# Optimization experiments

Hardware: AMD Instinct MI355X
Metric: run time of the kernel (lower is better)

Reference implementation:

```python
import jax, jax.numpy as jnp
import numpy as np

VNUMS = [4248, 4258, 5327, 3721, 5404, 2818]
B, C, H, W = 12, 64, 192, 192
DV, HID, BOX = 128, 256, 32


def _roi_patches(imgs, pros, imgbatch, box_len=BOX):
    # torchvision roi_align (aligned=False, sampling_ratio -> 1 sample per 1x1 bin):
    # bilinear sample at bin centers x1 + (j+0.5), y1 + (i+0.5)
    ar = jnp.arange(box_len, dtype=pros.dtype) + 0.5
    xs = pros[:, 0:1] - box_len / 2.0 + ar  # [G, box]
    ys = pros[:, 1:2] - box_len / 2.0 + ar  # [G, box]
    img_g = imgs[imgbatch]  # [G, C, H, W]

    def sample_one(img_chw, ys1, xs1):
        yy, xx = jnp.meshgrid(ys1, xs1, indexing="ij")  # [box, box]
        def per_c(ch):
            return jax.scipy.ndimage.map_coordinates(ch, [yy, xx], order=1, mode="nearest")
        return jax.vmap(per_c)(img_chw)  # [C, box, box]

    return jax.vmap(sample_one)(img_g, ys, xs)  # [G, C, box, box]


def setup_inputs() -> dict:
    key = jax.random.key(0)
    ks = jax.random.split(key, 6)
    G = 2 * B
    gtypes = np.array([(g // 2) % 6 if g % 2 == 0 else ((g // 2) + 3) % 6 for g in range(G)], dtype=np.int64)
    vnums_g = np.array([VNUMS[t] for t in gtypes])
    off = np.concatenate([[0], np.cumsum(vnums_g)])
    Nv = int(off[-1])  # 103104
    gar_of_vert = np.repeat(np.arange(G), vnums_g)
    idxs = []
    for t in range(6):
        gl = np.nonzero(gtypes == t)[0]
        idxs.append(np.concatenate([off[g] + np.arange(VNUMS[t]) for g in gl]).astype(np.int32))
    Din = DV + C
    pros = jax.random.uniform(ks[1], (G, 2), jnp.float32) * (H - 2.0 * BOX) + BOX
    inp = {
        "imgs": jax.random.normal(ks[0], (B, C, H, W), jnp.float32),
        "pros": pros,
        "x_verts": jax.random.normal(ks[2], (Nv, DV), jnp.float32),
        "W1": jax.random.normal(ks[3], (6, Din, HID), jnp.float32) / np.sqrt(Din).astype(np.float32),
        "W2": jax.random.normal(ks[4], (6, HID, HID), jnp.float32) / np.sqrt(HID).astype(np.float32),
        "W3": jax.random.normal(ks[5], (6, HID, 3), jnp.float32) / np.sqrt(HID).astype(np.float32),
        "imgbatch": jnp.asarray(np.arange(G) // 2, jnp.int32),
        "gar_of_vert": jnp.asarray(gar_of_vert, jnp.int32),
    }
    for t in range(6):
        inp[f"idx_t{t}"] = jnp.asarray(idxs[t])
    return inp


def reference(imgs, pros, x_verts, W1, W2, W3, imgbatch, gar_of_vert,
              idx_t0, idx_t1, idx_t2, idx_t3, idx_t4, idx_t5):
    # 1) roi_align patch extraction + pooled per-garment image feature
    patches = _roi_patches(imgs, pros, imgbatch)        # [G, C, 32, 32]
    garf = patches.mean(axis=(2, 3))                     # [G, C]
    # 2) per-vertex feature = [vertex feat | garment image feat]
    feat = jnp.concatenate([x_verts, garf[gar_of_vert]], axis=-1)  # [Nv, DV+C]
    # 3) MoE-style dispatch per garment type -> per-type expert MLP -> scatter-combine
    out = jnp.zeros((x_verts.shape[0], 3), feat.dtype)
    for t, idx in enumerate([idx_t0, idx_t1, idx_t2, idx_t3, idx_t4, idx_t5]):
        ft = feat[idx]                                   # gather (dispatch)
        h = jax.nn.relu(ft @ W1[t])
        h = jax.nn.relu(h @ W2[t])
        out = out.at[idx].set(h @ W3[t])                 # scatter (combine)
    return out
```

## Files before the change

### kernel.cpp

```cpp
#include <hip/hip_runtime.h>

typedef __attribute__((ext_vector_type(8))) short short8;
typedef __attribute__((ext_vector_type(4))) float float4_;

__device__ __forceinline__ unsigned short f2bf(float f) {
    unsigned u = __float_as_uint(f);
    u += 0x7FFFu + ((u >> 16) & 1u);
    return (unsigned short)(u >> 16);
}

#define GARF_BLOCKS 1536
#define PREP_BLOCKS 2784

__global__ void prep_garf(const float* __restrict__ imgs,
                          const float* __restrict__ pros,
                          const int* __restrict__ imgbatch,
                          const float* __restrict__ W1,
                          const float* __restrict__ W2,
                          const float* __restrict__ W3,
                          unsigned short* __restrict__ w1t,
                          unsigned short* __restrict__ w2t,
                          unsigned short* __restrict__ w3t,
                          float* __restrict__ garf) {
    const int tid = threadIdx.x;
    if (blockIdx.x < GARF_BLOCKS) {
        __shared__ float part[4];
        int pc = blockIdx.x;
        int g = pc >> 6, c = pc & 63;
        int b = imgbatch[g];
        float cx = pros[g * 2 + 0], cy = pros[g * 2 + 1];
        int i = tid >> 3;
        int j0 = (tid & 7) * 4;
        float y = cy - 16.0f + (float)i + 0.5f;
        float yf = floorf(y);
        float wy1 = y - yf, wy0 = 1.0f - wy1;
        int iy0 = min(max((int)yf, 0), 191), iy1 = min(max((int)yf + 1, 0), 191);
        const float* base = imgs + (size_t)(b * 64 + c) * 36864;
        const float* r0 = base + iy0 * 192;
        const float* r1 = base + iy1 * 192;
        float sum = 0.0f;
#pragma unroll
        for (int jj = 0; jj < 4; ++jj) {
            float x = cx - 16.0f + (float)(j0 + jj) + 0.5f;
            float xf = floorf(x);
            float wx1 = x - xf, wx0 = 1.0f - wx1;
            int ix0 = min(max((int)xf, 0), 191), ix1 = min(max((int)xf + 1, 0), 191);
            sum += wy0 * (wx0 * r0[ix0] + wx1 * r0[ix1]) +
                   wy1 * (wx0 * r1[ix0] + wx1 * r1[ix1]);
        }
        for (int s = 32; s >= 1; s >>= 1) sum += __shfl_xor(sum, s);
        if ((tid & 63) == 0) part[tid >> 6] = sum;
        __syncthreads();
        if (tid == 0)
            garf[g * 64 + c] = (part[0] + part[1] + part[2] + part[3]) * (1.0f / 1024.0f);
    } else {
        int id = (blockIdx.x - GARF_BLOCKS) * 256 + tid;
        if (id < 294912) {
            int t = id / 49152, r = id % 49152;
            int k = r >> 8, n = r & 255;
            w1t[t * 49152 + n * 192 + k] = f2bf(W1[id]);
        } else if (id < 688128) {
            int i2 = id - 294912;
            int t = i2 >> 16, r = i2 & 65535;
            int k = r >> 8, n = r & 255;
            w2t[t * 65536 + n * 256 + k] = f2bf(W2[i2]);
        } else if (id < 712704) {
            int i3 = id - 688128;
            int t = i3 >> 12, r = i3 & 4095;
            int n = r >> 8, k = r & 255;
            w3t[i3] = (n < 3) ? f2bf(W3[t * 768 + k * 3 + n]) : (unsigned short)0;
        }
    }
}

struct MoEArgs {
    const float* x_verts;
    const int* gar;
    const int* idx[6];
    const unsigned short* w1t;
    const unsigned short* w2t;
    const unsigned short* w3t;
    const float* garf;
    float* out;
    int cnt[6];
    int tile_end[6];
};

__global__ __launch_bounds__(512, 4) void moe_kernel(MoEArgs a) {
    __shared__ __align__(16) char smem[2][32768];

    const int tid = threadIdx.x;
    const int half = tid >> 8;
    const int ltid = tid & 255;
    char* sF = smem[half];

    const int total = a.tile_end[5];
    const int bt = blockIdx.x * 2 + half;
    const bool active = bt < total;

    int t = 0;
    if (active) { while (t < 5 && bt >= a.tile_end[t]) ++t; }
    const int tile = active ? (bt - (t ? a.tile_end[t - 1] : 0)) : 0;
    const int cnt = a.cnt[t];
    const int i0 = tile * 64;
    const int* idx = a.idx[t];

    const int lane = ltid & 63, w = ltid >> 6, q = lane >> 4, l = lane & 15;
    const unsigned short* w1 = a.w1t + (size_t)t * 49152;
    const unsigned short* w2 = a.w2t + (size_t)t * 65536;
    const unsigned short* w3 = a.w3t + (size_t)t * 4096;

    float4_ acc[4][4];

    auto STAGE = [&]() {
#pragma unroll
        for (int e0 = 0; e0 < 1536; e0 += 256) {
            int e = e0 + ltid;
            int m = e / 24, u = e - m * 24;
            int mi = i0 + m; mi = (mi < cnt) ? mi : (cnt - 1);
            int vid = idx[mi];
            const float* src = (u < 16)
                ? a.x_verts + (size_t)vid * 128 + u * 8
                : a.garf + (size_t)a.gar[vid] * 64 + (u - 16) * 8;
            float4 v0 = ((const float4*)src)[0];
            float4 v1 = ((const float4*)src)[1];
            short8 pk;
            pk[0] = f2bf(v0.x); pk[1] = f2bf(v0.y); pk[2] = f2bf(v0.z); pk[3] = f2bf(v0.w);
            pk[4] = f2bf(v1.x); pk[5] = f2bf(v1.y); pk[6] = f2bf(v1.z); pk[7] = f2bf(v1.w);
            *(short8*)(sF + m * 384 + ((u ^ (m & 7)) * 16)) = pk;
        }
    };

    auto C1 = [&]() {
#pragma unroll
        for (int mt = 0; mt < 4; ++mt)
#pragma unroll
            for (int nt = 0; nt < 4; ++nt) acc[mt][nt] = (float4_){0.f, 0.f, 0.f, 0.f};
        for (int ks = 0; ks < 6; ++ks) {
            short8 af[4], bfr[4];
#pragma unroll
            for (int mt = 0; mt < 4; ++mt)
                af[mt] = *(const short8*)(w1 + (w * 64 + mt * 16 + l) * 192 + ks * 32 + q * 8);
#pragma unroll
            for (int nt = 0; nt < 4; ++nt) {
                int v = nt * 16 + l;
                bfr[nt] = *(const short8*)(sF + v * 384 + (((ks * 4 + q) ^ (v & 7)) * 16));
            }
#pragma unroll
            for (int mt = 0; mt < 4; ++mt)
#pragma unroll
                for (int nt = 0; nt < 4; ++nt)
                    acc[mt][nt] = __builtin_amdgcn_mfma_f32_16x16x32_bf16(
                        af[mt], bfr[nt], acc[mt][nt], 0, 0, 0);
        }
    };

    auto EPI = [&]() {
#pragma unroll
        for (int mt = 0; mt < 4; ++mt)
#pragma unroll
            for (int nt = 0; nt < 4; ++nt) {
                int v = nt * 16 + l;
                int hu8 = w * 16 + mt * 4 + q;
                int ku16 = hu8 >> 1, par = hu8 & 1;
                uint2 pk;
                pk.x = (unsigned)f2bf(fmaxf(acc[mt][nt][0], 0.0f)) |
                       ((unsigned)f2bf(fmaxf(acc[mt][nt][1], 0.0f)) << 16);
                pk.y = (unsigned)f2bf(fmaxf(acc[mt][nt][2], 0.0f)) |
                       ((unsigned)f2bf(fmaxf(acc[mt][nt][3], 0.0f)) << 16);
                *(uint2*)(sF + v * 512 + ((ku16 ^ (v & 7)) * 16) + par * 8) = pk;
            }
    };

    auto C2 = [&]() {
#pragma unroll
        for (int mt = 0; mt < 4; ++mt)
#pragma unroll
            for (int nt = 0; nt < 4; ++nt) acc[mt][nt] = (float4_){0.f, 0.f, 0.f, 0.f};
        for (int ks = 0; ks < 8; ++ks) {
            short8 af[4], bfr[4];
#pragma unroll
            for (int mt = 0; mt < 4; ++mt)
                af[mt] = *(const short8*)(w2 + (w * 64 + mt * 16 + l) * 256 + ks * 32 + q * 8);
#pragma unroll
            for (int nt = 0; nt < 4; ++nt) {
                int v = nt * 16 + l;
                bfr[nt] = *(const short8*)(sF + v * 512 + (((ks * 4 + q) ^ (v & 7)) * 16));
            }
#pragma unroll
            for (int mt = 0; mt < 4; ++mt)
#pragma unroll
                for (int nt = 0; nt < 4; ++nt)
                    acc[mt][nt] = __builtin_amdgcn_mfma_f32_16x16x32_bf16(
                        af[mt], bfr[nt], acc[mt][nt], 0, 0, 0);
        }
    };

    auto C3 = [&]() {
        float4_ acc3 = (float4_){0.f, 0.f, 0.f, 0.f};
        int v3 = w * 16 + l;
        for (int ks = 0; ks < 8; ++ks) {
            short8 a3 = *(const short8*)(w3 + l * 256 + ks * 32 + q * 8);
            short8 b3 = *(const short8*)(sF + v3 * 512 + (((ks * 4 + q) ^ (v3 & 7)) * 16));
            acc3 = __builtin_amdgcn_mfma_f32_16x16x32_bf16(a3, b3, acc3, 0, 0, 0);
        }
        if (q == 0 && i0 + v3 < cnt) {
            float* o = a.out + (size_t)idx[i0 + v3] * 3;
            o[0] = acc3[0]; o[1] = acc3[1]; o[2] = acc3[2];
        }
    };

    if (half == 0) { if (active) STAGE(); }
    __syncthreads();
    if (half == 0) { if (active) C1(); } else { if (active) STAGE(); }
    __syncthreads();
    if (half == 0) { if (active) EPI(); } else { if (active) C1(); }
    __syncthreads();
    if (half == 0) { if (active) C2(); } else { if (active) EPI(); }
    __syncthreads();
    if (half == 0) { if (active) EPI(); } else { if (active) C2(); }
    __syncthreads();
    if (half == 0) { if (active) C3(); } else { if (active) EPI(); }
    __syncthreads();
    if (half == 1 && active) C3();
}

extern "C" void kernel_launch(void* const* d_in, const int* in_sizes, int n_in,
                              void* d_out, int out_size, void* d_ws, size_t ws_size,
                              hipStream_t stream) {
    const float* imgs    = (const float*)d_in[0];
    const float* pros    = (const float*)d_in[1];
    const float* x_verts = (const float*)d_in[2];
    const float* W1      = (const float*)d_in[3];
    const float* W2      = (const float*)d_in[4];
    const float* W3      = (const float*)d_in[5];
    const int* imgbatch  = (const int*)d_in[6];
    const int* gar       = (const int*)d_in[7];

    unsigned short* w1t = (unsigned short*)d_ws;
    unsigned short* w2t = (unsigned short*)((char*)d_ws + 589824);
    unsigned short* w3t = (unsigned short*)((char*)d_ws + 1376256);
    float* garf         = (float*)((char*)d_ws + 1425408);

    prep_garf<<<GARF_BLOCKS + PREP_BLOCKS, 256, 0, stream>>>(
        imgs, pros, imgbatch, W1, W2, W3, w1t, w2t, w3t, garf);

    MoEArgs a;
    a.x_verts = x_verts;
    a.gar = gar;
    for (int t = 0; t < 6; ++t) a.idx[t] = (const int*)d_in[8 + t];
    a.w1t = w1t; a.w2t = w2t; a.w3t = w3t;
    a.garf = garf;
    a.out = (float*)d_out;
    int tiles = 0;
    for (int t = 0; t < 6; ++t) {
        a.cnt[t] = in_sizes[8 + t];
        tiles += (a.cnt[t] + 63) / 64;
        a.tile_end[t] = tiles;
    }
    moe_kernel<<<(tiles + 1) / 2, 512, 0, stream>>>(a);
}
```

Before: 275.4 us.

## Convert MoE kernel to persistent single-tile blocks with prefetched gathers

Replaces the two-half ping-pong 512-thread block with a persistent 256-thread block that loops over tiles in a grid-strided fashion (up to 768 blocks). It prefetches the next tile's vertex indices and x_verts rows into registers during the current tile's GEMMs, and caches indices and garment ids in shared memory. The goal is to hide gather latency behind MFMA work and to cut launch and per-block overhead. In exchange it uses more registers for the prefetch buffers, adds extra barriers per tile, and lowers occupancy to 3 blocks per SIMD target.

```diff
diff --git a/kernel.cpp b/kernel.cpp
--- a/kernel.cpp
+++ b/kernel.cpp
@@ -86,74 +86,58 @@
     int tile_end[6];
 };
 
-__global__ __launch_bounds__(512, 4) void moe_kernel(MoEArgs a) {
-    __shared__ __align__(16) char smem[2][32768];
+__global__ __launch_bounds__(256, 3) void moe_kernel(MoEArgs a) {
+    __shared__ __align__(16) char smem[32768 + 1024];
+    char* sF = smem;
+    int* sidx0 = (int*)(smem + 32768);
+    int* sg0   = sidx0 + 64;
+    int* sidx1 = sg0 + 64;
+    int* sg1   = sidx1 + 64;
 
     const int tid = threadIdx.x;
-    const int half = tid >> 8;
-    const int ltid = tid & 255;
-    char* sF = smem[half];
-
     const int total = a.tile_end[5];
-    const int bt = blockIdx.x * 2 + half;
-    const bool active = bt < total;
-
-    int t = 0;
-    if (active) { while (t < 5 && bt >= a.tile_end[t]) ++t; }
-    const int tile = active ? (bt - (t ? a.tile_end[t - 1] : 0)) : 0;
-    const int cnt = a.cnt[t];
-    const int i0 = tile * 64;
-    const int* idx = a.idx[t];
-
-    const int lane = ltid & 63, w = ltid >> 6, q = lane >> 4, l = lane & 15;
-    const unsigned short* w1 = a.w1t + (size_t)t * 49152;
-    const unsigned short* w2 = a.w2t + (size_t)t * 65536;
-    const unsigned short* w3 = a.w3t + (size_t)t * 4096;
+    const int nb = gridDim.x;
+    int bt = blockIdx.x;
+    if (bt >= total) return;
+
+    const int lane = tid & 63, w = tid >> 6, q = lane >> 4, l = lane & 15;
+
+    auto resolve = [&](int b, int& t_, int& i0_, const int*& idx_, int& cnt_) {
+        int t = 0;
+        while (t < 5 && b >= a.tile_end[t]) ++t;
+        t_ = t;
+        i0_ = (b - (t ? a.tile_end[t - 1] : 0)) * 64;
+        idx_ = a.idx[t];
+        cnt_ = a.cnt[t];
+    };
+
+    int t, i0, cnt; const int* idx;
+    resolve(bt, t, i0, idx, cnt);
+
+    int* sA = sidx0; int* gA = sg0;
+    int* sB = sidx1; int* gB = sg1;
+
+    if (tid < 64) {
+        int m = i0 + tid; if (m > cnt - 1) m = cnt - 1;
+        int v = idx[m];
+        sA[tid] = v;
+        gA[tid] = a.gar[v];
+    }
+    __syncthreads();
+
+    float4 pfx[8];
+    {
+        int u = tid & 15;
+#pragma unroll
+        for (int k = 0; k < 4; ++k) {
+            int m = (tid >> 4) + k * 16;
+            const float* src = a.x_verts + (size_t)sA[m] * 128 + u * 8;
+            pfx[2 * k]     = ((const float4*)src)[0];
+            pfx[2 * k + 1] = ((const float4*)src)[1];
+        }
+    }
 
     float4_ acc[4][4];
-
-    auto STAGE = [&]() {
-#pragma unroll
-        for (int e0 = 0; e0 < 1536; e0 += 256) {
-            int e = e0 + ltid;
-            int m = e / 24, u = e - m * 24;
-            int mi = i0 + m; mi = (mi < cnt) ? mi : (cnt - 1);
-            int vid = idx[mi];
-            const float* src = (u < 16)
-                ? a.x_verts + (size_t)vid * 128 + u * 8
-                : a.garf + (size_t)a.gar[vid] * 64 + (u - 16) * 8;
-            float4 v0 = ((const float4*)src)[0];
-            float4 v1 = ((const float4*)src)[1];
-            short8 pk;
-            pk[0] = f2bf(v0.x); pk[1] = f2bf(v0.y); pk[2] = f2bf(v0.z); pk[3] = f2bf(v0.w);
-            pk[4] = f2bf(v1.x); pk[5] = f2bf(v1.y); pk[6] = f2bf(v1.z); pk[7] = f2bf(v1.w);
-            *(short8*)(sF + m * 384 + ((u ^ (m & 7)) * 16)) = pk;
-        }
-    };
-
-    auto C1 = [&]() {
-#pragma unroll
-        for (int mt = 0; mt < 4; ++mt)
-#pragma unroll
-            for (int nt = 0; nt < 4; ++nt) acc[mt][nt] = (float4_){0.f, 0.f, 0.f, 0.f};
-        for (int ks = 0; ks < 6; ++ks) {
-            short8 af[4], bfr[4];
-#pragma unroll
-            for (int mt = 0; mt < 4; ++mt)
-                af[mt] = *(const short8*)(w1 + (w * 64 + mt * 16 + l) * 192 + ks * 32 + q * 8);
-#pragma unroll
-            for (int nt = 0; nt < 4; ++nt) {
-                int v = nt * 16 + l;
-                bfr[nt] = *(const short8*)(sF + v * 384 + (((ks * 4 + q) ^ (v & 7)) * 16));
-            }
-#pragma unroll
-            for (int mt = 0; mt < 4; ++mt)
-#pragma unroll
-                for (int nt = 0; nt < 4; ++nt)
-                    acc[mt][nt] = __builtin_amdgcn_mfma_f32_16x16x32_bf16(
-                        af[mt], bfr[nt], acc[mt][nt], 0, 0, 0);
-        }
-    };
 
     auto EPI = [&]() {
 #pragma unroll
@@ -172,7 +156,98 @@
             }
     };
 
-    auto C2 = [&]() {
+    for (;;) {
+        const bool havenext = (bt + nb) < total;
+        int tN = 0, i0N = 0, cntN = 0; const int* idxN = nullptr;
+        if (havenext) resolve(bt + nb, tN, i0N, idxN, cntN);
+
+        float4 gf[4];
+        {
+#pragma unroll
+            for (int k = 0; k < 2; ++k) {
+                int m = (tid >> 3) + k * 32;
+                const float* src = a.garf + (size_t)gA[m] * 64 + (tid & 7) * 8;
+                gf[2 * k]     = ((const float4*)src)[0];
+                gf[2 * k + 1] = ((const float4*)src)[1];
+            }
+        }
+        int ridx = 0;
+        if (havenext && tid < 64) {
+            int m = i0N + tid; if (m > cntN - 1) m = cntN - 1;
+            ridx = idxN[m];
+        }
+        {
+            int u = tid & 15;
+#pragma unroll
+            for (int k = 0; k < 4; ++k) {
+                int m = (tid >> 4) + k * 16;
+                short8 pk;
+                pk[0] = f2bf(pfx[2 * k].x);     pk[1] = f2bf(pfx[2 * k].y);
+                pk[2] = f2bf(pfx[2 * k].z);     pk[3] = f2bf(pfx[2 * k].w);
+                pk[4] = f2bf(pfx[2 * k + 1].x); pk[5] = f2bf(pfx[2 * k + 1].y);
+                pk[6] = f2bf(pfx[2 * k + 1].z); pk[7] = f2bf(pfx[2 * k + 1].w);
+                *(short8*)(sF + m * 384 + ((u ^ (m & 7)) * 16)) = pk;
+            }
+        }
+        {
+            int u8 = tid & 7;
+#pragma unroll
+            for (int k = 0; k < 2; ++k) {
+                int m = (tid >> 3) + k * 32;
+                short8 pk;
+                pk[0] = f2bf(gf[2 * k].x);     pk[1] = f2bf(gf[2 * k].y);
+                pk[2] = f2bf(gf[2 * k].z);     pk[3] = f2bf(gf[2 * k].w);
+                pk[4] = f2bf(gf[2 * k + 1].x); pk[5] = f2bf(gf[2 * k + 1].y);
+                pk[6] = f2bf(gf[2 * k + 1].z); pk[7] = f2bf(gf[2 * k + 1].w);
+                *(short8*)(sF + m * 384 + (((16 + u8) ^ (m & 7)) * 16)) = pk;
+            }
+        }
+        __syncthreads();
+
+        const unsigned short* w1 = a.w1t + (size_t)t * 49152;
+#pragma unroll
+        for (int mt = 0; mt < 4; ++mt)
+#pragma unroll
+            for (int nt = 0; nt < 4; ++nt) acc[mt][nt] = (float4_){0.f, 0.f, 0.f, 0.f};
+        for (int ks = 0; ks < 6; ++ks) {
+            short8 af[4], bfr[4];
+#pragma unroll
+            for (int mt = 0; mt < 4; ++mt)
+                af[mt] = *(const short8*)(w1 + (w * 64 + mt * 16 + l) * 192 + ks * 32 + q * 8);
+#pragma unroll
+            for (int nt = 0; nt < 4; ++nt) {
+                int v = nt * 16 + l;
+                bfr[nt] = *(const short8*)(sF + v * 384 + (((ks * 4 + q) ^ (v & 7)) * 16));
+            }
+#pragma unroll
+            for (int mt = 0; mt < 4; ++mt)
+#pragma unroll
+                for (int nt = 0; nt < 4; ++nt)
+                    acc[mt][nt] = __builtin_amdgcn_mfma_f32_16x16x32_bf16(
+                        af[mt], bfr[nt], acc[mt][nt], 0, 0, 0);
+        }
+        int rgar = 0;
+        if (havenext && tid < 64) {
+            sB[tid] = ridx;
+            rgar = a.gar[ridx];
+        }
+        __syncthreads();
+
+        EPI();
+        if (havenext) {
+            int u = tid & 15;
+#pragma unroll
+            for (int k = 0; k < 4; ++k) {
+                int m = (tid >> 4) + k * 16;
+                const float* src = a.x_verts + (size_t)sB[m] * 128 + u * 8;
+                pfx[2 * k]     = ((const float4*)src)[0];
+                pfx[2 * k + 1] = ((const float4*)src)[1];
+            }
+            if (tid < 64) gB[tid] = rgar;
+        }
+        __syncthreads();
+
+        const unsigned short* w2 = a.w2t + (size_t)t * 65536;
 #pragma unroll
         for (int mt = 0; mt < 4; ++mt)
 #pragma unroll
@@ -194,35 +269,32 @@
                     acc[mt][nt] = __builtin_amdgcn_mfma_f32_16x16x32_bf16(
                         af[mt], bfr[nt], acc[mt][nt], 0, 0, 0);
         }
-    };
-
-    auto C3 = [&]() {
-        float4_ acc3 = (float4_){0.f, 0.f, 0.f, 0.f};
-        int v3 = w * 16 + l;
-        for (int ks = 0; ks < 8; ++ks) {
-            short8 a3 = *(const short8*)(w3 + l * 256 + ks * 32 + q * 8);
-            short8 b3 = *(const short8*)(sF + v3 * 512 + (((ks * 4 + q) ^ (v3 & 7)) * 16));
-            acc3 = __builtin_amdgcn_mfma_f32_16x16x32_bf16(a3, b3, acc3, 0, 0, 0);
-        }
-        if (q == 0 && i0 + v3 < cnt) {
-            float* o = a.out + (size_t)idx[i0 + v3] * 3;
-            o[0] = acc3[0]; o[1] = acc3[1]; o[2] = acc3[2];
-        }
-    };
-
-    if (half == 0) { if (active) STAGE(); }
-    __syncthreads();
-    if (half == 0) { if (active) C1(); } else { if (active) STAGE(); }
-    __syncthreads();
-    if (half == 0) { if (active) EPI(); } else { if (active) C1(); }
-    __syncthreads();
-    if (half == 0) { if (active) C2(); } else { if (active) EPI(); }
-    __syncthreads();
-    if (half == 0) { if (active) EPI(); } else { if (active) C2(); }
-    __syncthreads();
-    if (half == 0) { if (active) C3(); } else { if (active) EPI(); }
-    __syncthreads();
-    if (half == 1 && active) C3();
+        __syncthreads();
+
+        EPI();
+        __syncthreads();
+
+        {
+            float4_ acc3 = (float4_){0.f, 0.f, 0.f, 0.f};
+            const unsigned short* w3 = a.w3t + (size_t)t * 4096;
+            int v3 = w * 16 + l;
+            for (int ks = 0; ks < 8; ++ks) {
+                short8 a3 = *(const short8*)(w3 + l * 256 + ks * 32 + q * 8);
+                short8 b3 = *(const short8*)(sF + v3 * 512 + (((ks * 4 + q) ^ (v3 & 7)) * 16));
+                acc3 = __builtin_amdgcn_mfma_f32_16x16x32_bf16(a3, b3, acc3, 0, 0, 0);
+            }
+            if (q == 0 && i0 + v3 < cnt) {
+                float* o = a.out + (size_t)sA[v3] * 3;
+                o[0] = acc3[0]; o[1] = acc3[1]; o[2] = acc3[2];
+            }
+        }
+
+        if (!havenext) break;
+        bt += nb; t = tN; i0 = i0N; cnt = cntN; idx = idxN;
+        { int* tmp = sA; sA = sB; sB = tmp; }
+        { int* tmp = gA; gA = gB; gB = tmp; }
+        __syncthreads();
+    }
 }
 
 extern "C" void kernel_launch(void* const* d_in, const int* in_sizes, int n_in,
@@ -258,5 +330,6 @@
         tiles += (a.cnt[t] + 63) / 64;
         a.tile_end[t] = tiles;
     }
-    moe_kernel<<<(tiles + 1) / 2, 512, 0, stream>>>(a);
+    int nb = tiles < 768 ? tiles : 768;
+    moe_kernel<<<nb, 256, 0, stream>>>(a);
 }
```

New measurement: 279.4 us. About the same (+1.5%).

## Restructure MoE MLP to per-wavefront 16-vertex tiles without block barriers

Applied to the files above, without the earlier changes.

Replaces the two-half 64-vertex block pipeline with independent wavefronts, each processing 16 vertices through all three layers. Inputs are loaded directly into MFMA B-fragments from global memory, and a private 8KB LDS slice holds each wave's hidden activations, so __syncthreads is no longer needed. The goal is to drop barrier stalls and staging overhead. In exchange, each weight fragment is now reused across only 16 vertices instead of 64, so weight traffic from L2/global per vertex goes up fourfold.

```diff
diff --git a/kernel.cpp b/kernel.cpp
--- a/kernel.cpp
+++ b/kernel.cpp
@@ -86,143 +86,108 @@
     int tile_end[6];
 };
 
-__global__ __launch_bounds__(512, 4) void moe_kernel(MoEArgs a) {
-    __shared__ __align__(16) char smem[2][32768];
+__global__ __launch_bounds__(256, 4) void moe_kernel(MoEArgs a) {
+    __shared__ __align__(16) char smem[4][8192];
 
     const int tid = threadIdx.x;
-    const int half = tid >> 8;
-    const int ltid = tid & 255;
-    char* sF = smem[half];
-
-    const int total = a.tile_end[5];
-    const int bt = blockIdx.x * 2 + half;
-    const bool active = bt < total;
+    const int w = tid >> 6, lane = tid & 63, q = lane >> 4, l = lane & 15;
+    char* sW = smem[w];
+
+    int wt = blockIdx.x * 4 + w;
+    if (wt >= a.tile_end[5]) return;
 
     int t = 0;
-    if (active) { while (t < 5 && bt >= a.tile_end[t]) ++t; }
-    const int tile = active ? (bt - (t ? a.tile_end[t - 1] : 0)) : 0;
+    while (t < 5 && wt >= a.tile_end[t]) ++t;
+    const int i0 = (wt - (t ? a.tile_end[t - 1] : 0)) * 16;
     const int cnt = a.cnt[t];
-    const int i0 = tile * 64;
     const int* idx = a.idx[t];
 
-    const int lane = ltid & 63, w = ltid >> 6, q = lane >> 4, l = lane & 15;
+    int mi = i0 + l;
+    const bool valid = mi < cnt;
+    if (!valid) mi = cnt - 1;
+    const int vid = idx[mi];
+    const int garv = a.gar[vid];
+
     const unsigned short* w1 = a.w1t + (size_t)t * 49152;
     const unsigned short* w2 = a.w2t + (size_t)t * 65536;
     const unsigned short* w3 = a.w3t + (size_t)t * 4096;
 
-    float4_ acc[4][4];
-
-    auto STAGE = [&]() {
-#pragma unroll
-        for (int e0 = 0; e0 < 1536; e0 += 256) {
-            int e = e0 + ltid;
-            int m = e / 24, u = e - m * 24;
-            int mi = i0 + m; mi = (mi < cnt) ? mi : (cnt - 1);
-            int vid = idx[mi];
-            const float* src = (u < 16)
-                ? a.x_verts + (size_t)vid * 128 + u * 8
-                : a.garf + (size_t)a.gar[vid] * 64 + (u - 16) * 8;
-            float4 v0 = ((const float4*)src)[0];
-            float4 v1 = ((const float4*)src)[1];
-            short8 pk;
-            pk[0] = f2bf(v0.x); pk[1] = f2bf(v0.y); pk[2] = f2bf(v0.z); pk[3] = f2bf(v0.w);
-            pk[4] = f2bf(v1.x); pk[5] = f2bf(v1.y); pk[6] = f2bf(v1.z); pk[7] = f2bf(v1.w);
-            *(short8*)(sF + m * 384 + ((u ^ (m & 7)) * 16)) = pk;
-        }
-    };
-
-    auto C1 = [&]() {
-#pragma unroll
-        for (int mt = 0; mt < 4; ++mt)
-#pragma unroll
-            for (int nt = 0; nt < 4; ++nt) acc[mt][nt] = (float4_){0.f, 0.f, 0.f, 0.f};
-        for (int ks = 0; ks < 6; ++ks) {
-            short8 af[4], bfr[4];
-#pragma unroll
-            for (int mt = 0; mt < 4; ++mt)
-                af[mt] = *(const short8*)(w1 + (w * 64 + mt * 16 + l) * 192 + ks * 32 + q * 8);
-#pragma unroll
-            for (int nt = 0; nt < 4; ++nt) {
-                int v = nt * 16 + l;
-                bfr[nt] = *(const short8*)(sF + v * 384 + (((ks * 4 + q) ^ (v & 7)) * 16));
-            }
-#pragma unroll
-            for (int mt = 0; mt < 4; ++mt)
-#pragma unroll
-                for (int nt = 0; nt < 4; ++nt)
-                    acc[mt][nt] = __builtin_amdgcn_mfma_f32_16x16x32_bf16(
-                        af[mt], bfr[nt], acc[mt][nt], 0, 0, 0);
-        }
-    };
-
-    auto EPI = [&]() {
-#pragma unroll
-        for (int mt = 0; mt < 4; ++mt)
-#pragma unroll
-            for (int nt = 0; nt < 4; ++nt) {
-                int v = nt * 16 + l;
-                int hu8 = w * 16 + mt * 4 + q;
-                int ku16 = hu8 >> 1, par = hu8 & 1;
-                uint2 pk;
-                pk.x = (unsigned)f2bf(fmaxf(acc[mt][nt][0], 0.0f)) |
-                       ((unsigned)f2bf(fmaxf(acc[mt][nt][1], 0.0f)) << 16);
-                pk.y = (unsigned)f2bf(fmaxf(acc[mt][nt][2], 0.0f)) |
-                       ((unsigned)f2bf(fmaxf(acc[mt][nt][3], 0.0f)) << 16);
-                *(uint2*)(sF + v * 512 + ((ku16 ^ (v & 7)) * 16) + par * 8) = pk;
-            }
-    };
-
-    auto C2 = [&]() {
-#pragma unroll
-        for (int mt = 0; mt < 4; ++mt)
-#pragma unroll
-            for (int nt = 0; nt < 4; ++nt) acc[mt][nt] = (float4_){0.f, 0.f, 0.f, 0.f};
-        for (int ks = 0; ks < 8; ++ks) {
-            short8 af[4], bfr[4];
-#pragma unroll
-            for (int mt = 0; mt < 4; ++mt)
-                af[mt] = *(const short8*)(w2 + (w * 64 + mt * 16 + l) * 256 + ks * 32 + q * 8);
-#pragma unroll
-            for (int nt = 0; nt < 4; ++nt) {
-                int v = nt * 16 + l;
-                bfr[nt] = *(const short8*)(sF + v * 512 + (((ks * 4 + q) ^ (v & 7)) * 16));
-            }
-#pragma unroll
-            for (int mt = 0; mt < 4; ++mt)
-#pragma unroll
-                for (int nt = 0; nt < 4; ++nt)
-                    acc[mt][nt] = __builtin_amdgcn_mfma_f32_16x16x32_bf16(
-                        af[mt], bfr[nt], acc[mt][nt], 0, 0, 0);
-        }
-    };
-
-    auto C3 = [&]() {
-        float4_ acc3 = (float4_){0.f, 0.f, 0.f, 0.f};
-        int v3 = w * 16 + l;
-        for (int ks = 0; ks < 8; ++ks) {
-            short8 a3 = *(const short8*)(w3 + l * 256 + ks * 32 + q * 8);
-            short8 b3 = *(const short8*)(sF + v3 * 512 + (((ks * 4 + q) ^ (v3 & 7)) * 16));
-            acc3 = __builtin_amdgcn_mfma_f32_16x16x32_bf16(a3, b3, acc3, 0, 0, 0);
-        }
-        if (q == 0 && i0 + v3 < cnt) {
-            float* o = a.out + (size_t)idx[i0 + v3] * 3;
-            o[0] = acc3[0]; o[1] = acc3[1]; o[2] = acc3[2];
-        }
-    };
-
-    if (half == 0) { if (active) STAGE(); }
-    __syncthreads();
-    if (half == 0) { if (active) C1(); } else { if (active) STAGE(); }
-    __syncthreads();
-    if (half == 0) { if (active) EPI(); } else { if (active) C1(); }
-    __syncthreads();
-    if (half == 0) { if (active) C2(); } else { if (active) EPI(); }
-    __syncthreads();
-    if (half == 0) { if (active) EPI(); } else { if (active) C2(); }
-    __syncthreads();
-    if (half == 0) { if (active) C3(); } else { if (active) EPI(); }
-    __syncthreads();
-    if (half == 1 && active) C3();
+    float4_ acc[16] = {};
+#pragma unroll
+    for (int ks = 0; ks < 6; ++ks) {
+        const float* bsrc = (ks < 4)
+            ? a.x_verts + (size_t)vid * 128 + ks * 32 + q * 8
+            : a.garf + (size_t)garv * 64 + (ks - 4) * 32 + q * 8;
+        float4 v0 = ((const float4*)bsrc)[0];
+        float4 v1 = ((const float4*)bsrc)[1];
+        short8 bfr;
+        bfr[0] = f2bf(v0.x); bfr[1] = f2bf(v0.y); bfr[2] = f2bf(v0.z); bfr[3] = f2bf(v0.w);
+        bfr[4] = f2bf(v1.x); bfr[5] = f2bf(v1.y); bfr[6] = f2bf(v1.z); bfr[7] = f2bf(v1.w);
+#pragma unroll
+        for (int mg = 0; mg < 4; ++mg) {
+            short8 af[4];
+#pragma unroll
+            for (int i = 0; i < 4; ++i)
+                af[i] = *(const short8*)(w1 + (size_t)((mg * 4 + i) * 16 + l) * 192 + ks * 32 + q * 8);
+#pragma unroll
+            for (int i = 0; i < 4; ++i)
+                acc[mg * 4 + i] = __builtin_amdgcn_mfma_f32_16x16x32_bf16(
+                    af[i], bfr, acc[mg * 4 + i], 0, 0, 0);
+        }
+    }
+
+#pragma unroll
+    for (int mt = 0; mt < 16; ++mt) {
+        int hu8 = mt * 4 + q;
+        int ku16 = hu8 >> 1, par = hu8 & 1;
+        uint2 pk;
+        pk.x = (unsigned)f2bf(fmaxf(acc[mt][0], 0.0f)) |
+               ((unsigned)f2bf(fmaxf(acc[mt][1], 0.0f)) << 16);
+        pk.y = (unsigned)f2bf(fmaxf(acc[mt][2], 0.0f)) |
+               ((unsigned)f2bf(fmaxf(acc[mt][3], 0.0f)) << 16);
+        *(uint2*)(sW + l * 512 + ((ku16 ^ (l & 7)) * 16) + par * 8) = pk;
+    }
+
+    float4_ acc2[16] = {};
+#pragma unroll
+    for (int ks = 0; ks < 8; ++ks) {
+        short8 bfr = *(const short8*)(sW + l * 512 + (((ks * 4 + q) ^ (l & 7)) * 16));
+#pragma unroll
+        for (int mg = 0; mg < 4; ++mg) {
+            short8 af[4];
+#pragma unroll
+            for (int i = 0; i < 4; ++i)
+                af[i] = *(const short8*)(w2 + (size_t)((mg * 4 + i) * 16 + l) * 256 + ks * 32 + q * 8);
+#pragma unroll
+            for (int i = 0; i < 4; ++i)
+                acc2[mg * 4 + i] = __builtin_amdgcn_mfma_f32_16x16x32_bf16(
+                    af[i], bfr, acc2[mg * 4 + i], 0, 0, 0);
+        }
+    }
+
+#pragma unroll
+    for (int mt = 0; mt < 16; ++mt) {
+        int hu8 = mt * 4 + q;
+        int ku16 = hu8 >> 1, par = hu8 & 1;
+        uint2 pk;
+        pk.x = (unsigned)f2bf(fmaxf(acc2[mt][0], 0.0f)) |
+               ((unsigned)f2bf(fmaxf(acc2[mt][1], 0.0f)) << 16);
+        pk.y = (unsigned)f2bf(fmaxf(acc2[mt][2], 0.0f)) |
+               ((unsigned)f2bf(fmaxf(acc2[mt][3], 0.0f)) << 16);
+        *(uint2*)(sW + l * 512 + ((ku16 ^ (l & 7)) * 16) + par * 8) = pk;
+    }
+
+    float4_ acc3 = {};
+#pragma unroll
+    for (int ks = 0; ks < 8; ++ks) {
+        short8 a3 = *(const short8*)(w3 + l * 256 + ks * 32 + q * 8);
+        short8 b3 = *(const short8*)(sW + l * 512 + (((ks * 4 + q) ^ (l & 7)) * 16));
+        acc3 = __builtin_amdgcn_mfma_f32_16x16x32_bf16(a3, b3, acc3, 0, 0, 0);
+    }
+    if (q == 0 && valid) {
+        float* o = a.out + (size_t)vid * 3;
+        o[0] = acc3[0]; o[1] = acc3[1]; o[2] = acc3[2];
+    }
 }
 
 extern "C" void kernel_launch(void* const* d_in, const int* in_sizes, int n_in,
@@ -252,11 +217,11 @@
     a.w1t = w1t; a.w2t = w2t; a.w3t = w3t;
     a.garf = garf;
     a.out = (float*)d_out;
-    int tiles = 0;
+    int wtiles = 0;
     for (int t = 0; t < 6; ++t) {
         a.cnt[t] = in_sizes[8 + t];
-        tiles += (a.cnt[t] + 63) / 64;
-        a.tile_end[t] = tiles;
-    }
-    moe_kernel<<<(tiles + 1) / 2, 512, 0, stream>>>(a);
-}
+        wtiles += (a.cnt[t] + 15) / 16;
+        a.tile_end[t] = wtiles;
+    }
+    moe_kernel<<<(wtiles + 3) / 4, 256, 0, stream>>>(a);
+}
```

Measured after the change: 453.3 us. 1.65x slower.
